# Performance work log

Measured on AMD Instinct MI355X. Metric: run time of the kernel, lower is better.

## Reference

```python
import jax, jax.numpy as jnp
from jax import lax
import numpy as np


@jax.custom_vjp
def entmax15(x):
    return _entmax15_val(x)


def _entmax15_val(x):
    # 1.5-entmax along last axis (Peters et al. 2019), exact sort-based threshold
    x = (x - jnp.max(x, -1, keepdims=True)) / 2.0
    d = x.shape[-1]
    xs = -jnp.sort(-x, axis=-1)                      # descending
    rho = jnp.arange(1, d + 1, dtype=x.dtype)
    mean = jnp.cumsum(xs, -1) / rho
    mean_sq = jnp.cumsum(xs * xs, -1) / rho
    ss = rho * (mean_sq - mean * mean)
    delta = (1.0 - ss) / rho
    tau = mean - jnp.sqrt(jnp.clip(delta, 0.0))
    support = jnp.sum(tau <= xs, -1)
    tau_star = jnp.take_along_axis(tau, (support - 1)[..., None], -1)
    return jnp.square(jnp.clip(x - tau_star, 0.0))


def _entmax15_f(x):
    y = _entmax15_val(x)
    return y, y


def _entmax15_b(y, g):
    gppr = jnp.sqrt(y)                               # y^{2-alpha} with alpha=1.5
    dx = g * gppr
    q = jnp.sum(dx, -1, keepdims=True) / jnp.sum(gppr, -1, keepdims=True)
    return (dx - q * gppr,)


entmax15.defvjp(_entmax15_f, _entmax15_b)


def causal_conv(x, w, b, dilation):
    # x: [N, C_in, L]; left-pad (k-1)*dilation == conv+Chomp1d of the torch TCN
    pad = (w.shape[-1] - 1) * dilation
    y = lax.conv_general_dilated(x, w, (1,), [(pad, 0)], rhs_dilation=(dilation,),
                                 dimension_numbers=('NCH', 'OIH', 'NCH'))
    return y + b[None, :, None]


def temporal_block(x, w1, b1, w2, b2, wd, bd, dilation):
    h = jax.nn.relu(causal_conv(x, w1, b1, dilation))
    h = jax.nn.relu(causal_conv(h, w2, b2, dilation))
    res = x if wd is None else causal_conv(x, wd, bd, 1)  # 1x1 downsample
    return jax.nn.relu(h + res)


def _forward(src_seq, trg_seq,
             tcn0_w1, tcn0_b1, tcn0_w2, tcn0_b2, tcn0_wd, tcn0_bd,
             tcn1_w1, tcn1_b1, tcn1_w2, tcn1_b2,
             tcn2_w1, tcn2_b1, tcn2_w2, tcn2_b2,
             head1_w, head1_b, head2_w, head2_b):
    B, Ls, D = src_seq.shape
    Tp = trg_seq.shape[1]
    W = Ls + 1                                          # window = predict_start+1
    srctrg = jnp.concatenate([src_seq, trg_seq], axis=1)  # [B, Ls+Tp, D]
    # vectorized version of the python loop building in_conv (order: t-major, then batch)
    idx = jnp.arange(Tp)[:, None] + jnp.arange(W)[None, :]  # [Tp, W]
    win = srctrg[:, idx, :]                              # [B, Tp, W, D]
    x = win.transpose(1, 0, 3, 2).reshape(Tp * B, D, W)  # [N, D, W]
    x = temporal_block(x, tcn0_w1, tcn0_b1, tcn0_w2, tcn0_b2, tcn0_wd, tcn0_bd, 1)
    x = temporal_block(x, tcn1_w1, tcn1_b1, tcn1_w2, tcn1_b2, None, None, 2)
    x = temporal_block(x, tcn2_w1, tcn2_b1, tcn2_w2, tcn2_b2, None, None, 4)
    out = x.transpose(0, 2, 1)                           # [N, W, C]
    q = out[:, -1, :]                                    # [N, C]
    kv = out[:, :-1, :]                                  # [N, W-1, C]
    score = entmax15(jnp.einsum('nc,nlc->nl', q, kv))    # sparse attention weights
    c = jnp.einsum('nl,nlc->nc', score, kv)
    cc = jnp.concatenate([c, q], axis=-1)                # [N, 2C]
    y_hat = (cc @ head1_w.T + head1_b).reshape(Tp, B).T  # [B, Tp]
    sigma = jax.nn.softplus((cc @ head2_w.T + head2_b).reshape(Tp, B).T)
    return y_hat, sigma


def setup_inputs() -> dict:
    key = jax.random.key(0)
    ks = jax.random.split(key, 20)
    B, Ls, Tp, D, C, K = 128, 168, 24, 64, 128, 3
    n = lambda k, s: jax.random.normal(k, s, jnp.float32) * 0.05
    return {
        'src_seq': jax.random.normal(ks[0], (B, Ls, D), jnp.float32),
        'trg_seq': jax.random.normal(ks[1], (B, Tp, D), jnp.float32),
        'tcn0_w1': n(ks[2], (C, D, K)), 'tcn0_b1': n(ks[3], (C,)),
        'tcn0_w2': n(ks[4], (C, C, K)), 'tcn0_b2': n(ks[5], (C,)),
        'tcn0_wd': n(ks[6], (C, D, 1)), 'tcn0_bd': n(ks[7], (C,)),
        'tcn1_w1': n(ks[8], (C, C, K)), 'tcn1_b1': n(ks[9], (C,)),
        'tcn1_w2': n(ks[10], (C, C, K)), 'tcn1_b2': n(ks[11], (C,)),
        'tcn2_w1': n(ks[12], (C, C, K)), 'tcn2_b1': n(ks[13], (C,)),
        'tcn2_w2': n(ks[14], (C, C, K)), 'tcn2_b2': n(ks[15], (C,)),
        'head1_w': n(ks[16], (1, 2 * C)), 'head1_b': n(ks[17], (1,)),
        'head2_w': n(ks[18], (1, 2 * C)), 'head2_b': n(ks[19], (1,)),
    }


def reference(src_seq, trg_seq,
              tcn0_w1, tcn0_b1, tcn0_w2, tcn0_b2, tcn0_wd, tcn0_bd,
              tcn1_w1, tcn1_b1, tcn1_w2, tcn1_b2,
              tcn2_w1, tcn2_b1, tcn2_w2, tcn2_b2,
              head1_w, head1_b, head2_w, head2_b):
    return _forward(src_seq, trg_seq,
                    tcn0_w1, tcn0_b1, tcn0_w2, tcn0_b2, tcn0_wd, tcn0_bd,
                    tcn1_w1, tcn1_b1, tcn1_w2, tcn1_b2,
                    tcn2_w1, tcn2_b1, tcn2_w2, tcn2_b2,
                    head1_w, head1_b, head2_w, head2_b)
```

## Files before the change

### kernel.cpp

```cpp
#include <hip/hip_runtime.h>
#include <math.h>

typedef _Float16 f16;
typedef __attribute__((ext_vector_type(8))) _Float16 half8;
typedef __attribute__((ext_vector_type(2))) _Float16 half2v;
typedef __attribute__((ext_vector_type(4))) float f32x4;
typedef __attribute__((ext_vector_type(4))) float f4;

#define TPQ 24
#define BQ 128
#define LSQ 168

#if __has_builtin(__builtin_amdgcn_fdot2)
#define HAS_FDOT2 1
#else
#define HAS_FDOT2 0
#endif

#define E0 0
#define ED 24576
#define E1 32768
#define E2 81920
#define E3 131072
#define E4 180224
#define E5 229376
#define WTOT 278528
#define OG2 278528
#define OG1 3424256
#define OG0 4276224

#define MFMA16(a, b, c) __builtin_amdgcn_mfma_f32_16x16x32_f16((a), (b), (c), 0, 0, 0)

extern "C" __global__ void pack_weights(
    const float* __restrict__ w01, const float* __restrict__ wd0,
    const float* __restrict__ w02, const float* __restrict__ w11,
    const float* __restrict__ w12, const float* __restrict__ w21,
    const float* __restrict__ w22, f16* __restrict__ ws)
{
    int e = blockIdx.x * 256 + threadIdx.x;
    if (e >= WTOT) return;
    const float* W; int CIN, KK, el;
    if (e < ED) { W = w01; CIN = 64; KK = 3; el = e; }
    else if (e < E1) { W = wd0; CIN = 64; KK = 1; el = e - ED; }
    else {
        int c = (e - E1) / 49152; el = (e - E1) % 49152; CIN = 128; KK = 3;
        W = (c == 0) ? w02 : (c == 1) ? w11 : (c == 2) ? w12 : (c == 3) ? w21 : w22;
    }
    const int KB = CIN / 32;
    const int frag = el >> 9, wi = el & 511, lane = wi >> 3, i = wi & 7;
    const int coT = frag / (KK * KB), rem = frag % (KK * KB);
    const int kk = rem / KB, kb = rem % KB;
    const int co = coT * 16 + (lane & 15);
    const int ci = kb * 32 + (lane >> 4) * 8 + i;
    ws[e] = (f16)W[(co * CIN + ci) * KK + kk];
}

template<int CIN, int KK, int DIL, int RES, int RELU>
__device__ __forceinline__ void phaseA(
    const char* __restrict__ inb, char* __restrict__ outb,
    const f16* __restrict__ ws, int eoff, const float* __restrict__ bias, int tid)
{
    constexpr int KB = CIN / 32;
    constexpr int RB = CIN * 2;
    const int lane = tid & 63, wid = tid >> 6;
    const int cg = wid & 3, wg = wid >> 2;
    const int colr = lane & 15, quad = lane >> 4;
    const half8* __restrict__ wp = (const half8*)(ws + eoff);
    half8 wf[2][KK][KB];
#pragma unroll
    for (int ct = 0; ct < 2; ++ct)
#pragma unroll
        for (int kk = 0; kk < KK; ++kk)
#pragma unroll
            for (int kb = 0; kb < KB; ++kb)
                wf[ct][kk][kb] = wp[((((cg * 2 + ct) * KK) + kk) * KB + kb) * 64 + lane];
    const float bv0 = bias[cg * 32 + colr], bv1 = bias[cg * 32 + 16 + colr];
    const int t0 = wg ? 3 : 0, t1 = wg ? 5 : 3;
    for (int t = t0; t < t1; ++t) {
        const int w = t * 16 + colr;
        f32x4 a0 = {0.f, 0.f, 0.f, 0.f}, a1 = {0.f, 0.f, 0.f, 0.f};
#pragma unroll
        for (int kk = 0; kk < KK; ++kk) {
            const int r8 = w + 8 - (KK - 1 - kk) * DIL;
            const int rb = r8 * RB, sx = r8 & 7;
#pragma unroll
            for (int kb = 0; kb < KB; ++kb) {
                const half8 a = *(const half8*)(inb + rb + ((((kb * 4 + quad) ^ sx)) << 4));
                a0 = MFMA16(a, wf[0][kk][kb], a0);
                a1 = MFMA16(a, wf[1][kk][kb], a1);
            }
        }
#pragma unroll
        for (int ct = 0; ct < 2; ++ct) {
            const float bv = ct ? bv1 : bv0;
            const int co = cg * 32 + ct * 16 + colr;
#pragma unroll
            for (int j = 0; j < 4; ++j) {
                const int r8o = t * 16 + quad * 4 + j + 8;
                char* p = outb + r8o * 256 + ((((co >> 3) ^ (r8o & 7))) << 4) + ((co & 7) << 1);
                float v = (ct ? a1[j] : a0[j]) + bv;
                if (RELU) v = fmaxf(v, 0.f);
                if (RES)  v = fmaxf(v + (float)*(const f16*)p, 0.f);
                *(f16*)p = (f16)v;
            }
        }
    }
}

extern "C" __global__ void __launch_bounds__(512, 2)
tcn_global(const float* __restrict__ src, const float* __restrict__ trg,
           f16* __restrict__ ws,
           const float* __restrict__ b01, const float* __restrict__ bd0,
           const float* __restrict__ b02, const float* __restrict__ b11,
           const float* __restrict__ b12, const float* __restrict__ b21,
           const float* __restrict__ b22)
{
    __shared__ __align__(16) char sX[88 * 128];
    __shared__ __align__(16) char sH1[88 * 256];
    __shared__ __align__(16) char sH2[88 * 256];
    const int tid = threadIdx.x;
    const int b = blockIdx.x >> 2, chunk = blockIdx.x & 3;
    const int u0 = chunk * 48;
    const float* srcb = src + (size_t)b * LSQ * 64;
    const float* trgb = trg + (size_t)b * TPQ * 64;

    for (int e = tid; e < 80 * 8; e += 512) {
        const int w = e >> 3, gg = e & 7;
        const int p = u0 - 28 + w;
        half8 v = {};
        if (p >= 0 && p < 192) {
            const float* ptr = (p < 168) ? (srcb + p * 64 + gg * 8) : (trgb + (p - 168) * 64 + gg * 8);
            const f4 f0 = *(const f4*)ptr; const f4 f1 = *(const f4*)(ptr + 4);
            v[0] = (f16)f0[0]; v[1] = (f16)f0[1]; v[2] = (f16)f0[2]; v[3] = (f16)f0[3];
            v[4] = (f16)f1[0]; v[5] = (f16)f1[1]; v[6] = (f16)f1[2]; v[7] = (f16)f1[3];
        }
        const int r8 = w + 8;
        *(half8*)(sX + r8 * 128 + ((gg ^ (r8 & 7)) << 4)) = v;
    }
    if (tid < 320) {
        const half8 z = {};
        if (tid < 64)       *(half8*)(sX + tid * 16) = z;
        else if (tid < 192) *(half8*)(sH1 + (tid - 64) * 16) = z;
        else                *(half8*)(sH2 + (tid - 192) * 16) = z;
    }
    __syncthreads();

    phaseA<64, 3, 1, 0, 1>(sX, sH1, ws, E0, b01, tid);
    phaseA<64, 1, 1, 0, 0>(sX, sH2, ws, ED, bd0, tid);
    __syncthreads();
    phaseA<128, 3, 1, 1, 1>(sH1, sH2, ws, E1, b02, tid);
    __syncthreads();
    phaseA<128, 3, 2, 0, 1>(sH2, sH1, ws, E2, b11, tid);
    if (chunk == 0) {
        for (int e = tid; e < 36 * 16; e += 512) {
            const int p = e >> 4, gc = e & 15, r8 = p + 36;
            const half8 v = *(const half8*)(sH2 + r8 * 256 + ((gc ^ (r8 & 7)) << 4));
            *(half8*)(ws + OG0 + (size_t)(b * 36 + p) * 128 + gc * 8) = v;
        }
    }
    __syncthreads();
    phaseA<128, 3, 2, 1, 1>(sH1, sH2, ws, E3, b12, tid);
    __syncthreads();
    phaseA<128, 3, 4, 0, 1>(sH2, sH1, ws, E4, b21, tid);
    if (chunk == 0) {
        for (int e = tid; e < 52 * 16; e += 512) {
            const int p = e >> 4, gc = e & 15, r8 = p + 36;
            const half8 v = *(const half8*)(sH2 + r8 * 256 + ((gc ^ (r8 & 7)) << 4));
            *(half8*)(ws + OG1 + (size_t)(b * 52 + p) * 128 + gc * 8) = v;
        }
    }
    __syncthreads();
    phaseA<128, 3, 4, 1, 1>(sH1, sH2, ws, E5, b22, tid);
    __syncthreads();
    for (int e = tid; e < 48 * 16; e += 512) {
        const int pl = e >> 4, gc = e & 15, r8 = pl + 36;
        const int p = u0 + pl;
        const half8 v = *(const half8*)(sH2 + r8 * 256 + ((gc ^ (r8 & 7)) << 4));
        *(half8*)(ws + OG2 + (size_t)(b * 192 + p) * 128 + gc * 8) = v;
    }
}

template<int CIN, int KK, int DIL, int WPG, int SIN, int SOUT, int RES, int RELU>
__device__ __forceinline__ void bc_conv8(
    const char* __restrict__ inb, char* __restrict__ outb, const char* __restrict__ zrp,
    const f16* __restrict__ ws, int eoff, const float* __restrict__ bias, int tid)
{
    constexpr int KB = CIN / 32;
    constexpr int RB = CIN * 2;
    constexpr int NT = (4 * WPG) / 16;
    const int lane = tid & 63, wid = tid >> 6;
    const int colr = lane & 15, quad = lane >> 4;
    const half8* __restrict__ wp = (const half8*)(ws + eoff);
    half8 wf[KK][KB];
#pragma unroll
    for (int kk = 0; kk < KK; ++kk)
#pragma unroll
        for (int kb = 0; kb < KB; ++kb)
            wf[kk][kb] = wp[((wid * KK + kk) * KB + kb) * 64 + lane];
    const float bv = bias[wid * 16 + colr];
#pragma unroll
    for (int t = 0; t < NT; ++t) {
        const int m = t * 16 + colr;
        const int g = m / WPG, w = m - g * WPG;
        f32x4 aA = {0.f, 0.f, 0.f, 0.f}, aB = {0.f, 0.f, 0.f, 0.f};
#pragma unroll
        for (int kk = 0; kk < KK; ++kk) {
            const int wq = w - (KK - 1 - kk) * DIL;
            const int row = g * SIN + wq;
            const char* rb = (wq < 0) ? zrp : (inb + row * RB);
            const int sx = (wq < 0) ? 0 : (row & 7);
#pragma unroll
            for (int kb = 0; kb < KB; ++kb) {
                const half8 a = *(const half8*)(rb + ((((kb * 4 + quad) ^ sx)) << 4));
                if (kb & 1) aB = MFMA16(a, wf[kk][kb], aB);
                else        aA = MFMA16(a, wf[kk][kb], aA);
            }
        }
        const int co = wid * 16 + colr;
#pragma unroll
        for (int j = 0; j < 4; ++j) {
            const int mo = t * 16 + quad * 4 + j;
            const int go = mo / WPG, wo = mo - go * WPG;
            const int row = go * SOUT + wo;
            char* p = outb + row * 256 + ((((co >> 3) ^ (row & 7))) << 4) + ((co & 7) << 1);
            float v = aA[j] + aB[j] + bv;
            if (RELU) v = fmaxf(v, 0.f);
            if (RES)  v = fmaxf(v + (float)*(const f16*)p, 0.f);
            *(f16*)p = (f16)v;
        }
    }
}

__device__ __forceinline__ void bc_p2_8(
    const char* __restrict__ bx, const char* __restrict__ cb1, char* __restrict__ outB,
    const char* __restrict__ zrp, const f16* __restrict__ ws,
    const float* __restrict__ b02, const float* __restrict__ bd0, int tid)
{
    const int lane = tid & 63, wid = tid >> 6;
    const int colr = lane & 15, quad = lane >> 4;
    const half8* __restrict__ wpA = (const half8*)(ws + E1);
    const half8* __restrict__ wpD = (const half8*)(ws + ED);
    half8 wfa[3][4], wfd[2];
#pragma unroll
    for (int kk = 0; kk < 3; ++kk)
#pragma unroll
        for (int kb = 0; kb < 4; ++kb)
            wfa[kk][kb] = wpA[((wid * 3 + kk) * 4 + kb) * 64 + lane];
#pragma unroll
    for (int kb = 0; kb < 2; ++kb)
        wfd[kb] = wpD[(wid * 2 + kb) * 64 + lane];
    const float ba = b02[wid * 16 + colr];
    const float bd = bd0[wid * 16 + colr];
    const int g = colr >> 2, w = colr & 3;
    f32x4 aA = {0.f,0.f,0.f,0.f}, aB = {0.f,0.f,0.f,0.f};
    f32x4 dA = {0.f,0.f,0.f,0.f}, dB = {0.f,0.f,0.f,0.f};
#pragma unroll
    for (int kk = 0; kk < 3; ++kk) {
        const int wq = w - (2 - kk);
        const int row = g * 4 + wq;
        const char* rb = (wq < 0) ? zrp : (cb1 + row * 256);
        const int sx = (wq < 0) ? 0 : (row & 7);
#pragma unroll
        for (int kb = 0; kb < 4; ++kb) {
            const half8 a = *(const half8*)(rb + ((((kb * 4 + quad) ^ sx)) << 4));
            if (kb & 1) aB = MFMA16(a, wfa[kk][kb], aB);
            else        aA = MFMA16(a, wfa[kk][kb], aA);
        }
    }
    {
        const int row = g * 4 + w;
        const char* rb = bx + row * 128;
        const int sx = row & 7;
        const half8 x0 = *(const half8*)(rb + (((0 * 4 + quad) ^ sx) << 4));
        const half8 x1 = *(const half8*)(rb + (((1 * 4 + quad) ^ sx) << 4));
        dA = MFMA16(x0, wfd[0], dA);
        dB = MFMA16(x1, wfd[1], dB);
    }
    const int co = wid * 16 + colr;
#pragma unroll
    for (int j = 0; j < 4; ++j) {
        const int mo = quad * 4 + j;
        const int go = mo >> 2, wo = mo & 3;
        const int row = go * 28 + wo;
        char* p = outB + row * 256 + ((((co >> 3) ^ (row & 7))) << 4) + ((co & 7) << 1);
        const float ca = aA[j] + aB[j] + ba;
        const float cd = dA[j] + dB[j] + bd;
        *(f16*)p = (f16)fmaxf(fmaxf(ca, 0.f) + cd, 0.f);
    }
}

__device__ __forceinline__ float dot8(half8 kv, half8 vq, float s) {
#if HAS_FDOT2
#pragma unroll
    for (int j2 = 0; j2 < 4; ++j2) {
        half2v a = {kv[2 * j2], kv[2 * j2 + 1]};
        half2v q = {vq[2 * j2], vq[2 * j2 + 1]};
        s = __builtin_amdgcn_fdot2(a, q, s, false);
    }
#else
#pragma unroll
    for (int j = 0; j < 8; ++j) s = fmaf((float)kv[j], (float)vq[j], s);
#endif
    return s;
}

extern "C" __global__ void __launch_bounds__(512, 2)
tcn_bdattn(const float* __restrict__ src, const f16* __restrict__ ws,
           const float* __restrict__ b01, const float* __restrict__ bd0,
           const float* __restrict__ b02, const float* __restrict__ b11,
           const float* __restrict__ b12, const float* __restrict__ b21,
           const float* __restrict__ b22,
           const float* __restrict__ h1w, const float* __restrict__ h1b,
           const float* __restrict__ h2w, const float* __restrict__ h2b,
           float* __restrict__ out)
{
    __shared__ __align__(16) char BufB[112 * 256];
    __shared__ __align__(16) char BufC[112 * 256];
    __shared__ __align__(16) char sbx[16 * 128];
    __shared__ __align__(16) char scb1[16 * 256];
    __shared__ __align__(16) char zr[256];
    __shared__ __align__(16) f16 qh[512];
    __shared__ float qf[512];
    __shared__ float sc[672];
    __shared__ float xs[672];
    __shared__ float cvp[2][512];

    const int tid = threadIdx.x, lane = tid & 63, wid = tid >> 6;
    const int n0 = blockIdx.x << 2;
    const int tp = n0 >> 7, b0 = n0 & 127;

    if (tid < 16) *(half8*)(zr + tid * 16) = half8{};
    if (tid < 128) {
        const int g = tid >> 5, w = (tid >> 3) & 3, gg = tid & 7;
        const float* ptr = src + ((size_t)(b0 + g) * LSQ + (tp + w)) * 64 + gg * 8;
        const f4 f0 = *(const f4*)ptr; const f4 f1 = *(const f4*)(ptr + 4);
        half8 v;
        v[0] = (f16)f0[0]; v[1] = (f16)f0[1]; v[2] = (f16)f0[2]; v[3] = (f16)f0[3];
        v[4] = (f16)f1[0]; v[5] = (f16)f1[1]; v[6] = (f16)f1[2]; v[7] = (f16)f1[3];
        const int row = g * 4 + w;
        *(half8*)(sbx + row * 128 + ((gg ^ (row & 7)) << 4)) = v;
    }
    {
        const int e = tid;
        const int g = e >> 7, pw = 4 + ((e >> 4) & 7), gc = e & 15;
        const half8 v = *(const half8*)(ws + OG0 + (size_t)((b0 + g) * 36 + (tp + pw)) * 128 + gc * 8);
        const int row = g * 28 + pw;
        *(half8*)(BufB + row * 256 + ((gc ^ (row & 7)) << 4)) = v;
    }
    for (int e = tid; e < 1024; e += 512) {
        const int g = e >> 8, pw = 12 + ((e >> 4) & 15), gc = e & 15;
        const half8 v = *(const half8*)(ws + OG1 + (size_t)((b0 + g) * 52 + (tp + pw)) * 128 + gc * 8);
        const int row = g * 28 + pw;
        *(half8*)(BufB + row * 256 + ((gc ^ (row & 7)) << 4)) = v;
    }
    if (tid < 64) {
        const int g = tid >> 4, gc = tid & 15;
        const half8 v = *(const half8*)(ws + OG2 + (size_t)((b0 + g) * 192 + tp + 168) * 128 + gc * 8);
        *(half8*)(qh + g * 128 + gc * 8) = v;
#pragma unroll
        for (int j = 0; j < 8; ++j) qf[g * 128 + gc * 8 + j] = (float)v[j];
    }
    __syncthreads();

    bc_conv8<64, 3, 1, 4, 4, 4, 0, 1>(sbx, scb1, zr, ws, E0, b01, tid);
    __syncthreads();
    bc_p2_8(sbx, scb1, BufB, zr, ws, b02, bd0, tid);
    __syncthreads();
    bc_conv8<128, 3, 2, 12, 28, 28, 0, 1>(BufB, BufC, zr, ws, E2, b11, tid);
    __syncthreads();
    bc_conv8<128, 3, 2, 12, 28, 28, 1, 1>(BufC, BufB, zr, ws, E3, b12, tid);
    __syncthreads();
    bc_conv8<128, 3, 4, 28, 28, 28, 0, 1>(BufB, BufC, zr, ws, E4, b21, tid);
    __syncthreads();
    bc_conv8<128, 3, 4, 28, 28, 28, 1, 1>(BufC, BufB, zr, ws, E5, b22, tid);
    __syncthreads();

    const int g = wid >> 1, h = wid & 1;
    const int b = b0 + g;
    const f16* __restrict__ g2r = ws + OG2 + ((size_t)b * 192 + tp) * 128;
    const int wbase = h * 84;

#pragma unroll
    for (int it = 0; it < 2; ++it) {
        const int w = wbase + it * 64 + lane;
        if (it == 0 || lane < 20) {
            float s = 0.f;
            if (w < 28) {
                const int row = g * 28 + w, sx = row & 7;
                const char* rb = BufB + row * 256;
#pragma unroll
                for (int gc = 0; gc < 16; ++gc) {
                    const half8 kv = *(const half8*)(rb + ((gc ^ sx) << 4));
                    const half8 vq = *(const half8*)(qh + g * 128 + gc * 8);
                    s = dot8(kv, vq, s);
                }
            } else {
                const half8* rb = (const half8*)(g2r + (size_t)w * 128);
#pragma unroll
                for (int gc = 0; gc < 16; ++gc) {
                    const half8 kv = rb[gc];
                    const half8 vq = *(const half8*)(qh + g * 128 + gc * 8);
                    s = dot8(kv, vq, s);
                }
            }
            sc[g * 168 + w] = s;
        }
    }
    __syncthreads();

    {
        const int w0i = wbase + lane;
        const int w1i = wbase + 64 + lane;
        const float v0 = sc[g * 168 + w0i];
        const float v1 = (lane < 20) ? sc[g * 168 + w1i] : 0.f;
        int r0 = 0, r1 = 0;
        for (int m2 = 0; m2 < LSQ; ++m2) {
            const float u = sc[g * 168 + m2];
            r0 += (u > v0) || ((u == v0) && (m2 < w0i));
            r1 += (u > v1) || ((u == v1) && (m2 < w1i));
        }
        xs[g * 168 + r0] = v0;
        if (lane < 20) xs[g * 168 + r1] = v1;
    }
    __syncthreads();

    const float mx = xs[g * 168];
    float tau;
    {
        const int i0 = lane * 3;
        const float a0 = (i0     < LSQ) ? (xs[g * 168 + i0]     - mx) * 0.5f : 0.f;
        const float a1 = (i0 + 1 < LSQ) ? (xs[g * 168 + i0 + 1] - mx) * 0.5f : 0.f;
        const float a2 = (i0 + 2 < LSQ) ? (xs[g * 168 + i0 + 2] - mx) * 0.5f : 0.f;
        const float s1 = a0, s2 = a0 + a1, s3 = a0 + a1 + a2;
        const float q1 = a0 * a0, q2 = q1 + a1 * a1, q3 = q2 + a2 * a2;
        float ts = s3, tq = q3;
#pragma unroll
        for (int o = 1; o < 64; o <<= 1) {
            const float us = __shfl_up(ts, o);
            const float uq = __shfl_up(tq, o);
            if (lane >= o) { ts += us; tq += uq; }
        }
        const float eS = ts - s3, eQ = tq - q3;
        float tau0v, tau1v, tau2v; int ind = 0;
#define TAUC(CIDX, CS, CQ, AV, TVAR) { \
        const float rho = (float)(i0 + CIDX + 1); \
        const float mean = (CS) / rho; \
        const float msq = (CQ) / rho; \
        const float ssv = rho * (msq - mean * mean); \
        float delta = (1.f - ssv) / rho; \
        delta = delta > 0.f ? delta : 0.f; \
        TVAR = mean - sqrtf(delta); \
        if (i0 + CIDX < LSQ && TVAR <= (AV)) ++ind; }
        TAUC(0, eS + s1, eQ + q1, a0, tau0v)
        TAUC(1, eS + s2, eQ + q2, a1, tau1v)
        TAUC(2, eS + s3, eQ + q3, a2, tau2v)
#undef TAUC
#pragma unroll
        for (int o = 32; o; o >>= 1) ind += __shfl_xor(ind, o);
        const int sm1 = ind - 1;
        const int srcl = sm1 / 3, c = sm1 - srcl * 3;
        const float tsel = (c == 0) ? tau0v : (c == 1) ? tau1v : tau2v;
        tau = __shfl(tsel, srcl);
    }

    {
        const int c0 = lane * 2;
        float cv0 = 0.f, cv1 = 0.f;
#pragma unroll 4
        for (int wi = 0; wi < 84; ++wi) {
            const int w = wbase + wi;
            float pz = (sc[g * 168 + w] - mx) * 0.5f - tau;
            pz = fmaxf(pz, 0.f);
            const float pw = pz * pz;
            float k0, k1;
            if (w < 28) {
                const int row = g * 28 + w, sx = row & 7;
                const char* p = BufB + row * 256 + (((c0 >> 3) ^ sx) << 4) + ((c0 & 7) << 1);
                k0 = (float)*(const f16*)p;
                k1 = (float)*(const f16*)(p + 2);
            } else {
                const f16* p = g2r + (size_t)w * 128 + c0;
                k0 = (float)p[0];
                k1 = (float)p[1];
            }
            cv0 = fmaf(pw, k0, cv0);
            cv1 = fmaf(pw, k1, cv1);
        }
        cvp[h][g * 128 + c0] = cv0;
        cvp[h][g * 128 + c0 + 1] = cv1;
    }
    __syncthreads();

    if (h == 0) {
        const int c0 = lane * 2;
        const float cva = cvp[0][g * 128 + c0]     + cvp[1][g * 128 + c0];
        const float cvb = cvp[0][g * 128 + c0 + 1] + cvp[1][g * 128 + c0 + 1];
        const float q0 = qf[g * 128 + c0], q1 = qf[g * 128 + c0 + 1];
        float s1 = h1w[c0] * cva + h1w[c0 + 1] * cvb + h1w[128 + c0] * q0 + h1w[128 + c0 + 1] * q1;
        float s2 = h2w[c0] * cva + h2w[c0 + 1] * cvb + h2w[128 + c0] * q0 + h2w[128 + c0 + 1] * q1;
#pragma unroll
        for (int o = 32; o; o >>= 1) {
            s1 += __shfl_xor(s1, o);
            s2 += __shfl_xor(s2, o);
        }
        if (lane == 0) {
            const float y1 = s1 + h1b[0];
            const float z = s2 + h2b[0];
            const float sp = (z > 0.f) ? (z + log1pf(expf(-z))) : log1pf(expf(z));
            out[b * TPQ + tp] = y1;
            out[BQ * TPQ + b * TPQ + tp] = sp;
        }
    }
}

extern "C" void kernel_launch(void* const* d_in, const int* in_sizes, int n_in,
                              void* d_out, int out_size, void* d_ws, size_t ws_size,
                              hipStream_t stream) {
    const float* src = (const float*)d_in[0];
    const float* trg = (const float*)d_in[1];
    const float* w01 = (const float*)d_in[2];
    const float* b01 = (const float*)d_in[3];
    const float* w02 = (const float*)d_in[4];
    const float* b02 = (const float*)d_in[5];
    const float* wd0 = (const float*)d_in[6];
    const float* bd0 = (const float*)d_in[7];
    const float* w11 = (const float*)d_in[8];
    const float* b11 = (const float*)d_in[9];
    const float* w12 = (const float*)d_in[10];
    const float* b12 = (const float*)d_in[11];
    const float* w21 = (const float*)d_in[12];
    const float* b21 = (const float*)d_in[13];
    const float* w22 = (const float*)d_in[14];
    const float* b22 = (const float*)d_in[15];
    const float* h1w = (const float*)d_in[16];
    const float* h1b = (const float*)d_in[17];
    const float* h2w = (const float*)d_in[18];
    const float* h2b = (const float*)d_in[19];
    f16* ws = (f16*)d_ws;

    pack_weights<<<dim3((WTOT + 255) / 256), dim3(256), 0, stream>>>(
        w01, wd0, w02, w11, w12, w21, w22, ws);

    tcn_global<<<dim3(BQ * 4), dim3(512), 0, stream>>>(
        src, trg, ws, b01, bd0, b02, b11, b12, b21, b22);

    tcn_bdattn<<<dim3(TPQ * BQ / 4), dim3(512), 0, stream>>>(
        src, ws, b01, bd0, b02, b11, b12, b21, b22,
        h1w, h1b, h2w, h2b, (float*)d_out);
}
```

Baseline: 169.1 us.

## Halve tcn_bdattn blocks to two sequences with 256 threads and compact global stores

The attention/boundary kernel now processes two batch items per block with 256 threads instead of four with 512. Each wave computes two 16-channel output tiles in sequence, reloading weights per tile. Padded row strides of 32 and 16 replace 28 and 12, with a guard on the group index. The global kernel stores compacted intermediate buffers, skipping OG2 rows below 32 and splitting OG1 writes across chunks. This is meant to cut shared memory per block and raise occupancy and grid size. The cost is extra weight loads per wave and some wasted MFMA rows from padding.

```diff
diff --git a/kernel.cpp b/kernel.cpp
--- a/kernel.cpp
+++ b/kernel.cpp
@@ -26,8 +26,8 @@
 #define E5 229376
 #define WTOT 278528
 #define OG2 278528
-#define OG1 3424256
-#define OG0 4276224
+#define OG1 2899968
+#define OG0 3817472
 
 #define MFMA16(a, b, c) __builtin_amdgcn_mfma_f32_16x16x32_f16((a), (b), (c), 0, 0, 0)
 
@@ -152,10 +152,10 @@
     __syncthreads();
     phaseA<128, 3, 2, 0, 1>(sH2, sH1, ws, E2, b11, tid);
     if (chunk == 0) {
-        for (int e = tid; e < 36 * 16; e += 512) {
+        for (int e = tid; e < 40 * 16; e += 512) {
             const int p = e >> 4, gc = e & 15, r8 = p + 36;
             const half8 v = *(const half8*)(sH2 + r8 * 256 + ((gc ^ (r8 & 7)) << 4));
-            *(half8*)(ws + OG0 + (size_t)(b * 36 + p) * 128 + gc * 8) = v;
+            *(half8*)(ws + OG0 + (size_t)(b * 40 + p) * 128 + gc * 8) = v;
         }
     }
     __syncthreads();
@@ -163,10 +163,16 @@
     __syncthreads();
     phaseA<128, 3, 4, 0, 1>(sH2, sH1, ws, E4, b21, tid);
     if (chunk == 0) {
-        for (int e = tid; e < 52 * 16; e += 512) {
+        for (int e = tid; e < 48 * 16; e += 512) {
             const int p = e >> 4, gc = e & 15, r8 = p + 36;
             const half8 v = *(const half8*)(sH2 + r8 * 256 + ((gc ^ (r8 & 7)) << 4));
-            *(half8*)(ws + OG1 + (size_t)(b * 52 + p) * 128 + gc * 8) = v;
+            *(half8*)(ws + OG1 + (size_t)(b * 56 + p) * 128 + gc * 8) = v;
+        }
+    } else if (chunk == 1) {
+        for (int e = tid; e < 8 * 16; e += 512) {
+            const int p = 48 + (e >> 4), gc = e & 15, r8 = p - 12;
+            const half8 v = *(const half8*)(sH2 + r8 * 256 + ((gc ^ (r8 & 7)) << 4));
+            *(half8*)(ws + OG1 + (size_t)(b * 56 + p) * 128 + gc * 8) = v;
         }
     }
     __syncthreads();
@@ -175,63 +181,69 @@
     for (int e = tid; e < 48 * 16; e += 512) {
         const int pl = e >> 4, gc = e & 15, r8 = pl + 36;
         const int p = u0 + pl;
-        const half8 v = *(const half8*)(sH2 + r8 * 256 + ((gc ^ (r8 & 7)) << 4));
-        *(half8*)(ws + OG2 + (size_t)(b * 192 + p) * 128 + gc * 8) = v;
-    }
-}
-
-template<int CIN, int KK, int DIL, int WPG, int SIN, int SOUT, int RES, int RELU>
-__device__ __forceinline__ void bc_conv8(
+        if (p >= 32) {
+            const half8 v = *(const half8*)(sH2 + r8 * 256 + ((gc ^ (r8 & 7)) << 4));
+            *(half8*)(ws + OG2 + (size_t)(b * 160 + (p - 32)) * 128 + gc * 8) = v;
+        }
+    }
+}
+
+template<int CIN, int KK, int DIL, int WPG, int SIN, int SOUT, int RES, int RELU, int NT>
+__device__ __forceinline__ void bc_conv(
     const char* __restrict__ inb, char* __restrict__ outb, const char* __restrict__ zrp,
     const f16* __restrict__ ws, int eoff, const float* __restrict__ bias, int tid)
 {
     constexpr int KB = CIN / 32;
     constexpr int RB = CIN * 2;
-    constexpr int NT = (4 * WPG) / 16;
     const int lane = tid & 63, wid = tid >> 6;
     const int colr = lane & 15, quad = lane >> 4;
     const half8* __restrict__ wp = (const half8*)(ws + eoff);
-    half8 wf[KK][KB];
-#pragma unroll
-    for (int kk = 0; kk < KK; ++kk)
-#pragma unroll
-        for (int kb = 0; kb < KB; ++kb)
-            wf[kk][kb] = wp[((wid * KK + kk) * KB + kb) * 64 + lane];
-    const float bv = bias[wid * 16 + colr];
-#pragma unroll
-    for (int t = 0; t < NT; ++t) {
-        const int m = t * 16 + colr;
-        const int g = m / WPG, w = m - g * WPG;
-        f32x4 aA = {0.f, 0.f, 0.f, 0.f}, aB = {0.f, 0.f, 0.f, 0.f};
-#pragma unroll
-        for (int kk = 0; kk < KK; ++kk) {
-            const int wq = w - (KK - 1 - kk) * DIL;
-            const int row = g * SIN + wq;
-            const char* rb = (wq < 0) ? zrp : (inb + row * RB);
-            const int sx = (wq < 0) ? 0 : (row & 7);
-#pragma unroll
-            for (int kb = 0; kb < KB; ++kb) {
-                const half8 a = *(const half8*)(rb + ((((kb * 4 + quad) ^ sx)) << 4));
-                if (kb & 1) aB = MFMA16(a, wf[kk][kb], aB);
-                else        aA = MFMA16(a, wf[kk][kb], aA);
-            }
-        }
-        const int co = wid * 16 + colr;
-#pragma unroll
-        for (int j = 0; j < 4; ++j) {
-            const int mo = t * 16 + quad * 4 + j;
-            const int go = mo / WPG, wo = mo - go * WPG;
-            const int row = go * SOUT + wo;
-            char* p = outb + row * 256 + ((((co >> 3) ^ (row & 7))) << 4) + ((co & 7) << 1);
-            float v = aA[j] + aB[j] + bv;
-            if (RELU) v = fmaxf(v, 0.f);
-            if (RES)  v = fmaxf(v + (float)*(const f16*)p, 0.f);
-            *(f16*)p = (f16)v;
-        }
-    }
-}
-
-__device__ __forceinline__ void bc_p2_8(
+#pragma unroll
+    for (int ct = 0; ct < 2; ++ct) {
+        half8 wf[KK][KB];
+#pragma unroll
+        for (int kk = 0; kk < KK; ++kk)
+#pragma unroll
+            for (int kb = 0; kb < KB; ++kb)
+                wf[kk][kb] = wp[((((wid * 2 + ct) * KK) + kk) * KB + kb) * 64 + lane];
+        const float bv = bias[wid * 32 + ct * 16 + colr];
+#pragma unroll
+        for (int t = 0; t < NT; ++t) {
+            const int m = t * 16 + colr;
+            const int g = m / WPG, w = m - g * WPG;
+            f32x4 aA = {0.f, 0.f, 0.f, 0.f}, aB = {0.f, 0.f, 0.f, 0.f};
+#pragma unroll
+            for (int kk = 0; kk < KK; ++kk) {
+                const int wq = w - (KK - 1 - kk) * DIL;
+                const int row = g * SIN + wq;
+                const char* rb = (wq < 0) ? zrp : (inb + row * RB);
+                const int sx = (wq < 0) ? 0 : (row & 7);
+#pragma unroll
+                for (int kb = 0; kb < KB; ++kb) {
+                    const half8 a = *(const half8*)(rb + ((((kb * 4 + quad) ^ sx)) << 4));
+                    if (kb & 1) aB = MFMA16(a, wf[kk][kb], aB);
+                    else        aA = MFMA16(a, wf[kk][kb], aA);
+                }
+            }
+            const int co = wid * 32 + ct * 16 + colr;
+#pragma unroll
+            for (int j = 0; j < 4; ++j) {
+                const int mo = t * 16 + quad * 4 + j;
+                const int go = mo / WPG, wo = mo - go * WPG;
+                if (go < 2) {
+                    const int row = go * SOUT + wo;
+                    char* p = outb + row * 256 + ((((co >> 3) ^ (row & 7))) << 4) + ((co & 7) << 1);
+                    float v = aA[j] + aB[j] + bv;
+                    if (RELU) v = fmaxf(v, 0.f);
+                    if (RES)  v = fmaxf(v + (float)*(const f16*)p, 0.f);
+                    *(f16*)p = (f16)v;
+                }
+            }
+        }
+    }
+}
+
+__device__ __forceinline__ void bc_p2(
     const char* __restrict__ bx, const char* __restrict__ cb1, char* __restrict__ outB,
     const char* __restrict__ zrp, const f16* __restrict__ ws,
     const float* __restrict__ b02, const float* __restrict__ bd0, int tid)
@@ -240,52 +252,57 @@
     const int colr = lane & 15, quad = lane >> 4;
     const half8* __restrict__ wpA = (const half8*)(ws + E1);
     const half8* __restrict__ wpD = (const half8*)(ws + ED);
-    half8 wfa[3][4], wfd[2];
-#pragma unroll
-    for (int kk = 0; kk < 3; ++kk)
-#pragma unroll
-        for (int kb = 0; kb < 4; ++kb)
-            wfa[kk][kb] = wpA[((wid * 3 + kk) * 4 + kb) * 64 + lane];
-#pragma unroll
-    for (int kb = 0; kb < 2; ++kb)
-        wfd[kb] = wpD[(wid * 2 + kb) * 64 + lane];
-    const float ba = b02[wid * 16 + colr];
-    const float bd = bd0[wid * 16 + colr];
-    const int g = colr >> 2, w = colr & 3;
-    f32x4 aA = {0.f,0.f,0.f,0.f}, aB = {0.f,0.f,0.f,0.f};
-    f32x4 dA = {0.f,0.f,0.f,0.f}, dB = {0.f,0.f,0.f,0.f};
-#pragma unroll
-    for (int kk = 0; kk < 3; ++kk) {
-        const int wq = w - (2 - kk);
-        const int row = g * 4 + wq;
-        const char* rb = (wq < 0) ? zrp : (cb1 + row * 256);
-        const int sx = (wq < 0) ? 0 : (row & 7);
-#pragma unroll
-        for (int kb = 0; kb < 4; ++kb) {
-            const half8 a = *(const half8*)(rb + ((((kb * 4 + quad) ^ sx)) << 4));
-            if (kb & 1) aB = MFMA16(a, wfa[kk][kb], aB);
-            else        aA = MFMA16(a, wfa[kk][kb], aA);
-        }
-    }
-    {
-        const int row = g * 4 + w;
-        const char* rb = bx + row * 128;
-        const int sx = row & 7;
-        const half8 x0 = *(const half8*)(rb + (((0 * 4 + quad) ^ sx) << 4));
-        const half8 x1 = *(const half8*)(rb + (((1 * 4 + quad) ^ sx) << 4));
-        dA = MFMA16(x0, wfd[0], dA);
-        dB = MFMA16(x1, wfd[1], dB);
-    }
-    const int co = wid * 16 + colr;
-#pragma unroll
-    for (int j = 0; j < 4; ++j) {
-        const int mo = quad * 4 + j;
-        const int go = mo >> 2, wo = mo & 3;
-        const int row = go * 28 + wo;
-        char* p = outB + row * 256 + ((((co >> 3) ^ (row & 7))) << 4) + ((co & 7) << 1);
-        const float ca = aA[j] + aB[j] + ba;
-        const float cd = dA[j] + dB[j] + bd;
-        *(f16*)p = (f16)fmaxf(fmaxf(ca, 0.f) + cd, 0.f);
+#pragma unroll
+    for (int ct = 0; ct < 2; ++ct) {
+        half8 wfa[3][4], wfd[2];
+#pragma unroll
+        for (int kk = 0; kk < 3; ++kk)
+#pragma unroll
+            for (int kb = 0; kb < 4; ++kb)
+                wfa[kk][kb] = wpA[((((wid * 2 + ct) * 3) + kk) * 4 + kb) * 64 + lane];
+#pragma unroll
+        for (int kb = 0; kb < 2; ++kb)
+            wfd[kb] = wpD[((wid * 2 + ct) * 2 + kb) * 64 + lane];
+        const float ba = b02[wid * 32 + ct * 16 + colr];
+        const float bd = bd0[wid * 32 + ct * 16 + colr];
+        const int g = colr >> 2, w = colr & 3;
+        f32x4 aA = {0.f,0.f,0.f,0.f}, aB = {0.f,0.f,0.f,0.f};
+        f32x4 dA = {0.f,0.f,0.f,0.f}, dB = {0.f,0.f,0.f,0.f};
+#pragma unroll
+        for (int kk = 0; kk < 3; ++kk) {
+            const int wq = w - (2 - kk);
+            const int row = g * 4 + wq;
+            const char* rb = (wq < 0) ? zrp : (cb1 + row * 256);
+            const int sx = (wq < 0) ? 0 : (row & 7);
+#pragma unroll
+            for (int kb = 0; kb < 4; ++kb) {
+                const half8 a = *(const half8*)(rb + ((((kb * 4 + quad) ^ sx)) << 4));
+                if (kb & 1) aB = MFMA16(a, wfa[kk][kb], aB);
+                else        aA = MFMA16(a, wfa[kk][kb], aA);
+            }
+        }
+        {
+            const int row = g * 4 + w;
+            const char* rb = bx + row * 128;
+            const int sx = row & 7;
+            const half8 x0 = *(const half8*)(rb + (((0 * 4 + quad) ^ sx) << 4));
+            const half8 x1 = *(const half8*)(rb + (((1 * 4 + quad) ^ sx) << 4));
+            dA = MFMA16(x0, wfd[0], dA);
+            dB = MFMA16(x1, wfd[1], dB);
+        }
+        const int co = wid * 32 + ct * 16 + colr;
+#pragma unroll
+        for (int j = 0; j < 4; ++j) {
+            const int mo = quad * 4 + j;
+            const int go = mo >> 2, wo = mo & 3;
+            if (go < 2) {
+                const int row = go * 32 + wo;
+                char* p = outB + row * 256 + ((((co >> 3) ^ (row & 7))) << 4) + ((co & 7) << 1);
+                const float ca = aA[j] + aB[j] + ba;
+                const float cd = dA[j] + dB[j] + bd;
+                *(f16*)p = (f16)fmaxf(fmaxf(ca, 0.f) + cd, 0.f);
+            }
+        }
     }
 }
 
@@ -304,7 +321,7 @@
     return s;
 }
 
-extern "C" __global__ void __launch_bounds__(512, 2)
+extern "C" __global__ void __launch_bounds__(256, 2)
 tcn_bdattn(const float* __restrict__ src, const f16* __restrict__ ws,
            const float* __restrict__ b01, const float* __restrict__ bd0,
            const float* __restrict__ b02, const float* __restrict__ b11,
@@ -314,23 +331,23 @@
            const float* __restrict__ h2w, const float* __restrict__ h2b,
            float* __restrict__ out)
 {
-    __shared__ __align__(16) char BufB[112 * 256];
-    __shared__ __align__(16) char BufC[112 * 256];
-    __shared__ __align__(16) char sbx[16 * 128];
-    __shared__ __align__(16) char scb1[16 * 256];
+    __shared__ __align__(16) char BufB[64 * 256];
+    __shared__ __align__(16) char BufC[64 * 256];
     __shared__ __align__(16) char zr[256];
-    __shared__ __align__(16) f16 qh[512];
-    __shared__ float qf[512];
-    __shared__ float sc[672];
-    __shared__ float xs[672];
-    __shared__ float cvp[2][512];
+    __shared__ __align__(16) f16 qh[256];
+    __shared__ float qf[256];
+    __shared__ float sc[336];
+    __shared__ float xs[336];
+    __shared__ float cvp[2][2][128];
+    char* scb1 = BufC;
+    char* sbx  = BufC + 2048;
 
     const int tid = threadIdx.x, lane = tid & 63, wid = tid >> 6;
-    const int n0 = blockIdx.x << 2;
+    const int n0 = blockIdx.x << 1;
     const int tp = n0 >> 7, b0 = n0 & 127;
 
     if (tid < 16) *(half8*)(zr + tid * 16) = half8{};
-    if (tid < 128) {
+    if (tid < 64) {
         const int g = tid >> 5, w = (tid >> 3) & 3, gg = tid & 7;
         const float* ptr = src + ((size_t)(b0 + g) * LSQ + (tp + w)) * 64 + gg * 8;
         const f4 f0 = *(const f4*)ptr; const f4 f1 = *(const f4*)(ptr + 4);
@@ -340,44 +357,45 @@
         const int row = g * 4 + w;
         *(half8*)(sbx + row * 128 + ((gg ^ (row & 7)) << 4)) = v;
     }
-    {
-        const int e = tid;
-        const int g = e >> 7, pw = 4 + ((e >> 4) & 7), gc = e & 15;
-        const half8 v = *(const half8*)(ws + OG0 + (size_t)((b0 + g) * 36 + (tp + pw)) * 128 + gc * 8);
-        const int row = g * 28 + pw;
+    for (int e = tid; e < 384; e += 256) {
+        const int gc = e & 15, q = e >> 4;
+        const int g = q / 12, pw = 4 + (q - g * 12);
+        const half8 v = *(const half8*)(ws + OG0 + (size_t)((b0 + g) * 40 + (tp + pw)) * 128 + gc * 8);
+        const int row = g * 32 + pw;
         *(half8*)(BufB + row * 256 + ((gc ^ (row & 7)) << 4)) = v;
     }
-    for (int e = tid; e < 1024; e += 512) {
-        const int g = e >> 8, pw = 12 + ((e >> 4) & 15), gc = e & 15;
-        const half8 v = *(const half8*)(ws + OG1 + (size_t)((b0 + g) * 52 + (tp + pw)) * 128 + gc * 8);
-        const int row = g * 28 + pw;
+    for (int e = tid; e < 512; e += 256) {
+        const int gc = e & 15, q = e >> 4;
+        const int g = q >> 4, pw = 16 + (q & 15);
+        const half8 v = *(const half8*)(ws + OG1 + (size_t)((b0 + g) * 56 + (tp + pw)) * 128 + gc * 8);
+        const int row = g * 32 + pw;
         *(half8*)(BufB + row * 256 + ((gc ^ (row & 7)) << 4)) = v;
     }
-    if (tid < 64) {
+    if (tid < 32) {
         const int g = tid >> 4, gc = tid & 15;
-        const half8 v = *(const half8*)(ws + OG2 + (size_t)((b0 + g) * 192 + tp + 168) * 128 + gc * 8);
+        const half8 v = *(const half8*)(ws + OG2 + ((size_t)(b0 + g) * 160 + tp + 136) * 128 + gc * 8);
         *(half8*)(qh + g * 128 + gc * 8) = v;
 #pragma unroll
         for (int j = 0; j < 8; ++j) qf[g * 128 + gc * 8 + j] = (float)v[j];
     }
     __syncthreads();
 
-    bc_conv8<64, 3, 1, 4, 4, 4, 0, 1>(sbx, scb1, zr, ws, E0, b01, tid);
-    __syncthreads();
-    bc_p2_8(sbx, scb1, BufB, zr, ws, b02, bd0, tid);
-    __syncthreads();
-    bc_conv8<128, 3, 2, 12, 28, 28, 0, 1>(BufB, BufC, zr, ws, E2, b11, tid);
-    __syncthreads();
-    bc_conv8<128, 3, 2, 12, 28, 28, 1, 1>(BufC, BufB, zr, ws, E3, b12, tid);
-    __syncthreads();
-    bc_conv8<128, 3, 4, 28, 28, 28, 0, 1>(BufB, BufC, zr, ws, E4, b21, tid);
-    __syncthreads();
-    bc_conv8<128, 3, 4, 28, 28, 28, 1, 1>(BufC, BufB, zr, ws, E5, b22, tid);
+    bc_conv<64, 3, 1, 4, 4, 4, 0, 1, 1>(sbx, scb1, zr, ws, E0, b01, tid);
+    __syncthreads();
+    bc_p2(sbx, scb1, BufB, zr, ws, b02, bd0, tid);
+    __syncthreads();
+    bc_conv<128, 3, 2, 16, 32, 32, 0, 1, 2>(BufB, BufC, zr, ws, E2, b11, tid);
+    __syncthreads();
+    bc_conv<128, 3, 2, 16, 32, 32, 1, 1, 2>(BufC, BufB, zr, ws, E3, b12, tid);
+    __syncthreads();
+    bc_conv<128, 3, 4, 32, 32, 32, 0, 1, 4>(BufB, BufC, zr, ws, E4, b21, tid);
+    __syncthreads();
+    bc_conv<128, 3, 4, 32, 32, 32, 1, 1, 4>(BufC, BufB, zr, ws, E5, b22, tid);
     __syncthreads();
 
     const int g = wid >> 1, h = wid & 1;
     const int b = b0 + g;
-    const f16* __restrict__ g2r = ws + OG2 + ((size_t)b * 192 + tp) * 128;
+    const f16* __restrict__ g2r = ws + OG2 + ((size_t)b * 160 + tp - 32) * 128;
     const int wbase = h * 84;
 
 #pragma unroll
@@ -385,8 +403,8 @@
         const int w = wbase + it * 64 + lane;
         if (it == 0 || lane < 20) {
             float s = 0.f;
-            if (w < 28) {
-                const int row = g * 28 + w, sx = row & 7;
+            if (w < 32) {
+                const int row = g * 32 + w, sx = row & 7;
                 const char* rb = BufB + row * 256;
 #pragma unroll
                 for (int gc = 0; gc < 16; ++gc) {
@@ -473,8 +491,8 @@
             pz = fmaxf(pz, 0.f);
             const float pw = pz * pz;
             float k0, k1;
-            if (w < 28) {
-                const int row = g * 28 + w, sx = row & 7;
+            if (w < 32) {
+                const int row = g * 32 + w, sx = row & 7;
                 const char* p = BufB + row * 256 + (((c0 >> 3) ^ sx) << 4) + ((c0 & 7) << 1);
                 k0 = (float)*(const f16*)p;
                 k1 = (float)*(const f16*)(p + 2);
@@ -486,15 +504,15 @@
             cv0 = fmaf(pw, k0, cv0);
             cv1 = fmaf(pw, k1, cv1);
         }
-        cvp[h][g * 128 + c0] = cv0;
-        cvp[h][g * 128 + c0 + 1] = cv1;
+        cvp[h][g][c0] = cv0;
+        cvp[h][g][c0 + 1] = cv1;
     }
     __syncthreads();
 
     if (h == 0) {
         const int c0 = lane * 2;
-        const float cva = cvp[0][g * 128 + c0]     + cvp[1][g * 128 + c0];
-        const float cvb = cvp[0][g * 128 + c0 + 1] + cvp[1][g * 128 + c0 + 1];
+        const float cva = cvp[0][g][c0]     + cvp[1][g][c0];
+        const float cvb = cvp[0][g][c0 + 1] + cvp[1][g][c0 + 1];
         const float q0 = qf[g * 128 + c0], q1 = qf[g * 128 + c0 + 1];
         float s1 = h1w[c0] * cva + h1w[c0 + 1] * cvb + h1w[128 + c0] * q0 + h1w[128 + c0 + 1] * q1;
         float s2 = h2w[c0] * cva + h2w[c0 + 1] * cvb + h2w[128 + c0] * q0 + h2w[128 + c0 + 1] * q1;
@@ -544,7 +562,7 @@
     tcn_global<<<dim3(BQ * 4), dim3(512), 0, stream>>>(
         src, trg, ws, b01, bd0, b02, b11, b12, b21, b22);
 
-    tcn_bdattn<<<dim3(TPQ * BQ / 4), dim3(512), 0, stream>>>(
+    tcn_bdattn<<<dim3(TPQ * BQ / 2), dim3(256), 0, stream>>>(
         src, ws, b01, bd0, b02, b11, b12, b21, b22,
         h1w, h1b, h2w, h2b, (float*)d_out);
 }
```

Measured after the change: 161.4 us (median of 6 runs). 4.5% less time.
